# Kernel optimization log

Hardware: AMD Instinct MI355X
Metric: run time of the kernel (lower is better)

Reference implementation:

```python
import jax, jax.numpy as jnp
import numpy as np

NUM_EXPERTS = 3
INPUT_DIM = 1024
HIDDEN_DIM = 4096
OUTPUT_DIM = 1024
ROUTER_HIDDEN = 128
BATCH = 8192


def setup_inputs() -> dict:
    key = jax.random.key(0)
    ks = jax.random.split(key, 6)
    s_in = 1.0 / np.sqrt(INPUT_DIM)
    s_h = 1.0 / np.sqrt(HIDDEN_DIM)
    s_rh = 1.0 / np.sqrt(ROUTER_HIDDEN)
    return {
        "x": jax.random.normal(ks[0], (BATCH, INPUT_DIM), jnp.float32),
        "router_w1": jax.random.normal(ks[1], (INPUT_DIM, ROUTER_HIDDEN), jnp.float32) * s_in,
        "router_b1": jnp.zeros((ROUTER_HIDDEN,), jnp.float32),
        "router_w2": jax.random.normal(ks[2], (ROUTER_HIDDEN, NUM_EXPERTS), jnp.float32) * s_rh,
        "router_b2": jnp.zeros((NUM_EXPERTS,), jnp.float32),
        "expert_w1": jax.random.normal(ks[3], (NUM_EXPERTS, INPUT_DIM, HIDDEN_DIM), jnp.float32) * s_in,
        "expert_b1": jnp.zeros((NUM_EXPERTS, HIDDEN_DIM), jnp.float32),
        "expert_w2": jax.random.normal(ks[4], (NUM_EXPERTS, HIDDEN_DIM, OUTPUT_DIM), jnp.float32) * s_h,
        "expert_b2": jnp.zeros((NUM_EXPERTS, OUTPUT_DIM), jnp.float32),
    }


def reference(x, router_w1, router_b1, router_w2, router_b2,
              expert_w1, expert_b1, expert_w2, expert_b2):
    # Router: MLP -> softmax probs, hard top-1 selection (argmax)
    rh = jax.nn.relu(x @ router_w1 + router_b1)          # [B, 128]
    logits = rh @ router_w2 + router_b2                   # [B, E]
    probs = jax.nn.softmax(logits, axis=-1)
    selected = jnp.argmax(probs, axis=-1)                 # [B] int

    # Per-expert forward on all tokens (dense equivalent of masked dispatch)
    h = jax.nn.relu(jnp.einsum('bi,eih->ebh', x, expert_w1) + expert_b1[:, None, :])  # [E,B,H]
    y = jnp.einsum('ebh,eho->ebo', h, expert_w2) + expert_b2[:, None, :]              # [E,B,O]

    # Scatter-combine: each token takes its selected expert's output
    outputs = jnp.take_along_axis(
        y, selected[None, :, None], axis=0)[0]            # [B, O]

    # routing_stats: tokens per expert
    routing_stats = jnp.bincount(selected, length=NUM_EXPERTS)
    return outputs, routing_stats
```

## Files before the change

kernel.cpp:

```cpp
#include <hip/hip_runtime.h>
#include <hip/hip_bf16.h>

typedef short bf16x8 __attribute__((ext_vector_type(8)));
typedef float f32x4 __attribute__((ext_vector_type(4)));
typedef __attribute__((address_space(1))) const void gconst_t;
typedef __attribute__((address_space(3))) void lds_t;

#define DEVI __device__ __forceinline__

constexpr int BATCH   = 8192;
constexpr int IN_DIM  = 1024;
constexpr int HID     = 4096;
constexpr int OUT_DIM = 1024;
constexpr int NE      = 3;

constexpr size_t XBF_OFF  = 0;
constexpr size_t W1T_OFF  = 16777216;
constexpr size_t W2T_OFF  = W1T_OFF + 25165824;
constexpr size_t H_OFF    = W2T_OFF + 25165824;
constexpr size_t META_OFF = H_OFF + 67108864;

DEVI unsigned short f2bf(float f) {
  __hip_bfloat16 h = __float2bfloat16(f);
  return *reinterpret_cast<unsigned short*>(&h);
}

__global__ __launch_bounds__(256) void prep_kernel(
    const float* __restrict__ x, const float* __restrict__ ew1, const float* __restrict__ ew2,
    const float* __restrict__ rw1, const float* __restrict__ rb1,
    const float* __restrict__ rw2, const float* __restrict__ rb2,
    unsigned short* __restrict__ xb, unsigned short* __restrict__ w1t,
    unsigned short* __restrict__ w2t, int* __restrict__ counts, int* __restrict__ toklist) {
  __shared__ float smem[5184];
  const int b = blockIdx.x;
  const int tid = threadIdx.x;

  if (b < 1024) {
    const int t0 = b * 8;
    float* xs = smem;
    float* rh = smem + 4096;
    const int hcol = tid & 127;
    const int g = tid >> 7;
    float acc[4] = {0.f, 0.f, 0.f, 0.f};
    for (int half = 0; half < 2; half++) {
      __syncthreads();
      {
        const float* xsrc = x + (size_t)t0 * 1024 + half * 512;
        for (int i = tid; i < 1024; i += 256) {
          const int tok = i >> 7, c4 = i & 127;
          *(float4*)&xs[tok * 512 + c4 * 4] =
              *(const float4*)(xsrc + (size_t)tok * 1024 + c4 * 4);
        }
      }
      __syncthreads();
      const int kbase = half * 512;
      for (int k = 0; k < 512; k += 4) {
        const float w0 = rw1[(kbase + k + 0) * 128 + hcol];
        const float w1v = rw1[(kbase + k + 1) * 128 + hcol];
        const float w2v = rw1[(kbase + k + 2) * 128 + hcol];
        const float w3v = rw1[(kbase + k + 3) * 128 + hcol];
#pragma unroll
        for (int tt = 0; tt < 4; tt++) {
          const float4 xv = *(const float4*)&xs[(g * 4 + tt) * 512 + k];
          acc[tt] = fmaf(xv.x, w0, acc[tt]);
          acc[tt] = fmaf(xv.y, w1v, acc[tt]);
          acc[tt] = fmaf(xv.z, w2v, acc[tt]);
          acc[tt] = fmaf(xv.w, w3v, acc[tt]);
        }
      }
    }
    const float bb1 = rb1[hcol];
#pragma unroll
    for (int tt = 0; tt < 4; tt++)
      rh[(g * 4 + tt) * 132 + hcol] = fmaxf(acc[tt] + bb1, 0.f);
    __syncthreads();
    float* lg = smem + 4096 + 8 * 132;
    if (tid < 24) {
      const int t = tid / 3, e = tid % 3;
      float s = rb2[e];
      for (int j = 0; j < 128; j++) s = fmaf(rh[t * 132 + j], rw2[j * 3 + e], s);
      lg[t * 3 + e] = s;
    }
    __syncthreads();
    if (tid < 8) {
      const float l0 = lg[tid * 3], l1 = lg[tid * 3 + 1], l2 = lg[tid * 3 + 2];
      int sel = 0; float m = l0;
      if (l1 > m) { m = l1; sel = 1; }
      if (l2 > m) { m = l2; sel = 2; }
      const int slot = atomicAdd(&counts[sel], 1);
      toklist[sel * BATCH + slot] = t0 + tid;
    }
  } else if (b < 7168) {
    float (*tile)[65] = (float(*)[65])smem;
    const float* src; unsigned short* dst; int R, C, r0, c0;
    if (b < 4096) {
      const int bb = b - 1024, e = bb / 1024, w = bb % 1024;
      src = ew1 + (size_t)e * 1024 * 4096; dst = w1t + (size_t)e * 4096 * 1024;
      R = 1024; C = 4096; r0 = (w & 15) * 64; c0 = (w >> 4) * 64;
    } else {
      const int bb = b - 4096, e = bb / 1024, w = bb % 1024;
      src = ew2 + (size_t)e * 4096 * 1024; dst = w2t + (size_t)e * 1024 * 4096;
      R = 4096; C = 1024; r0 = (w & 63) * 64; c0 = (w >> 6) * 64;
    }
    const int tr = tid >> 4;
    const int tc = (tid & 15) << 2;
#pragma unroll
    for (int i = 0; i < 4; i++) {
      const int r = tr + i * 16;
      const float4 v = *(const float4*)(src + (size_t)(r0 + r) * C + (c0 + tc));
      tile[r][tc + 0] = v.x; tile[r][tc + 1] = v.y; tile[r][tc + 2] = v.z; tile[r][tc + 3] = v.w;
    }
    __syncthreads();
#pragma unroll
    for (int i = 0; i < 4; i++) {
      const int c = tr + i * 16;
      ushort4 o;
      o.x = f2bf(tile[tc + 0][c]);
      o.y = f2bf(tile[tc + 1][c]);
      o.z = f2bf(tile[tc + 2][c]);
      o.w = f2bf(tile[tc + 3][c]);
      *(ushort4*)(dst + (size_t)(c0 + c) * R + (r0 + tc)) = o;
    }
  } else {
    const float4* xv4 = (const float4*)x;
    const int total = BATCH * IN_DIM / 4;
    for (int i = (b - 7168) * 256 + tid; i < total; i += 512 * 256) {
      const float4 v = xv4[i];
      ushort4 o;
      o.x = f2bf(v.x); o.y = f2bf(v.y); o.z = f2bf(v.z); o.w = f2bf(v.w);
      ((ushort4*)xb)[i] = o;
    }
  }
}

template <int MODE>
__global__ __launch_bounds__(512, 2) void moe_gemm(
    const unsigned short* __restrict__ Abase, const unsigned short* __restrict__ Ball,
    const float* __restrict__ biasAll, unsigned short* __restrict__ Hout,
    float* __restrict__ Yout, const int* __restrict__ toklist, const int* __restrict__ counts,
    float* __restrict__ tail) {
  constexpr int N  = (MODE == 0) ? HID : OUT_DIM;
  constexpr int K  = (MODE == 0) ? IN_DIM : HID;
  constexpr int NT = K / 32;

  const int tid = threadIdx.x;
  if (MODE == 0 && blockIdx.x == 0 && blockIdx.y == 0 && tid < NE)
    tail[tid] = (float)counts[tid];

  const int c0 = counts[0], c1 = counts[1], c2 = counts[2];
  const int mb0 = (c0 + 127) >> 7, mb1 = (c1 + 127) >> 7, mb2 = (c2 + 127) >> 7;
  const int bx = blockIdx.x;
  int e, mblk;
  if (bx < mb0) { e = 0; mblk = bx; }
  else if (bx < mb0 + mb1) { e = 1; mblk = bx - mb0; }
  else if (bx < mb0 + mb1 + mb2) { e = 2; mblk = bx - mb0 - mb1; }
  else return;
  const int cnt = (e == 0) ? c0 : (e == 1) ? c1 : c2;
  const int m0 = mblk * 128;
  const int n0 = blockIdx.y * 256;
  const int off_e = (e > 0 ? c0 : 0) + (e > 1 ? c1 : 0);
  const unsigned short* Bmat = Ball + (size_t)e * ((size_t)N * K);
  const float* bias = biasAll + (size_t)e * N;

  __shared__ unsigned short Ab[3][128 * 32];
  __shared__ unsigned short Bb[3][256 * 32];

  const unsigned short* asrc;
  const unsigned short* bsrc[2];
  unsigned aoff, boff[2];
  {
    const unsigned o = (unsigned)tid * 16u;
    const unsigned p = o ^ (((o >> 6) & 3u) << 4);
    const int row = (int)(o >> 6);
    const int kel = (int)((p & 63u) >> 1);
    aoff = o;
    int slot = m0 + row; if (slot > cnt - 1) slot = cnt - 1;
    const size_t arow = (MODE == 0) ? (size_t)toklist[e * BATCH + slot]
                                    : (size_t)(off_e + slot);
    asrc = Abase + arow * K + kel;
  }
#pragma unroll
  for (int l = 0; l < 2; l++) {
    const unsigned o = l * 8192u + (unsigned)tid * 16u;
    const unsigned p = o ^ (((o >> 6) & 3u) << 4);
    const int row = (int)(o >> 6);
    const int kel = (int)((p & 63u) >> 1);
    boff[l] = o;
    bsrc[l] = Bmat + (size_t)(n0 + row) * K + kel;
  }

  f32x4 acc[4][4];
#pragma unroll
  for (int i = 0; i < 4; i++)
#pragma unroll
    for (int j = 0; j < 4; j++) acc[i][j] = {0.f, 0.f, 0.f, 0.f};

  const int lane = tid & 63;
  const int wave = tid >> 6;
  const int wm = (wave >> 2) * 64;
  const int wn = (wave & 3) * 64;
  const int fr = lane & 15;
  const int fc = lane >> 4;

  auto STAGE = [&](int buf, int kofs) {
    __builtin_amdgcn_global_load_lds((gconst_t*)(asrc + kofs),
                                     (lds_t*)((char*)&Ab[buf][0] + aoff), 16, 0, 0);
#pragma unroll
    for (int l = 0; l < 2; l++)
      __builtin_amdgcn_global_load_lds((gconst_t*)(bsrc[l] + kofs),
                                       (lds_t*)((char*)&Bb[buf][0] + boff[l]), 16, 0, 0);
  };

  STAGE(0, 0);
  STAGE(1, 32);

  int cur = 0;
  for (int t = 0; t < NT; ++t) {
    if (t + 1 < NT) asm volatile("s_waitcnt vmcnt(3)" ::: "memory");
    else            asm volatile("s_waitcnt vmcnt(0)" ::: "memory");
    __builtin_amdgcn_sched_barrier(0);
    __builtin_amdgcn_s_barrier();
    __builtin_amdgcn_sched_barrier(0);
    bf16x8 af[4], bv[4];
#pragma unroll
    for (int m = 0; m < 4; m++) {
      const unsigned row = (unsigned)(wm + m * 16 + fr);
      const unsigned addr = ((row << 6) + (unsigned)(fc << 4)) ^ ((row & 3u) << 4);
      af[m] = *(const bf16x8*)((const char*)&Ab[cur][0] + addr);
    }
#pragma unroll
    for (int n = 0; n < 4; n++) {
      const unsigned row = (unsigned)(wn + n * 16 + fr);
      const unsigned addr = ((row << 6) + (unsigned)(fc << 4)) ^ ((row & 3u) << 4);
      bv[n] = *(const bf16x8*)((const char*)&Bb[cur][0] + addr);
    }
    asm volatile("s_waitcnt lgkmcnt(0)" ::: "memory");
    __builtin_amdgcn_sched_barrier(0);
    __builtin_amdgcn_s_setprio(1);
#pragma unroll
    for (int m = 0; m < 4; m++)
#pragma unroll
      for (int n = 0; n < 4; n++)
        acc[m][n] = __builtin_amdgcn_mfma_f32_16x16x32_bf16(af[m], bv[n], acc[m][n], 0, 0, 0);
    __builtin_amdgcn_s_setprio(0);
    if (t + 2 < NT) {
      const int nb = (cur + 2 >= 3) ? cur - 1 : cur + 2;
      STAGE(nb, (t + 2) * 32);
    }
    cur = (cur + 1 == 3) ? 0 : cur + 1;
  }

  const int crow = (lane >> 4) * 4;
  const int ccol = lane & 15;
#pragma unroll
  for (int mi = 0; mi < 4; mi++) {
#pragma unroll
    for (int r = 0; r < 4; r++) {
      const int slot = m0 + wm + mi * 16 + crow + r;
      if (slot >= cnt) continue;
      if (MODE == 0) {
        unsigned short* hrow = Hout + (size_t)(off_e + slot) * HID;
#pragma unroll
        for (int ni = 0; ni < 4; ni++) {
          const int n = n0 + wn + ni * 16 + ccol;
          const float v = acc[mi][ni][r] + bias[n];
          hrow[n] = f2bf(fmaxf(v, 0.f));
        }
      } else {
        const int tok = toklist[e * BATCH + slot];
        float* yrow = Yout + (size_t)tok * OUT_DIM;
#pragma unroll
        for (int ni = 0; ni < 4; ni++) {
          const int n = n0 + wn + ni * 16 + ccol;
          yrow[n] = acc[mi][ni][r] + bias[n];
        }
      }
    }
  }
}

extern "C" void kernel_launch(void* const* d_in, const int* in_sizes, int n_in,
                              void* d_out, int out_size, void* d_ws, size_t ws_size,
                              hipStream_t stream) {
  const float* x   = (const float*)d_in[0];
  const float* rw1 = (const float*)d_in[1];
  const float* rb1 = (const float*)d_in[2];
  const float* rw2 = (const float*)d_in[3];
  const float* rb2 = (const float*)d_in[4];
  const float* ew1 = (const float*)d_in[5];
  const float* eb1 = (const float*)d_in[6];
  const float* ew2 = (const float*)d_in[7];
  const float* eb2 = (const float*)d_in[8];
  float* out = (float*)d_out;

  char* ws = (char*)d_ws;
  unsigned short* xb  = (unsigned short*)(ws + XBF_OFF);
  unsigned short* w1t = (unsigned short*)(ws + W1T_OFF);
  unsigned short* w2t = (unsigned short*)(ws + W2T_OFF);
  unsigned short* h   = (unsigned short*)(ws + H_OFF);
  int* counts  = (int*)(ws + META_OFF);
  int* toklist = counts + 16;
  float* tail = out + (size_t)BATCH * OUT_DIM;

  hipMemsetAsync(counts, 0, 64, stream);
  prep_kernel<<<7680, 256, 0, stream>>>(x, ew1, ew2, rw1, rb1, rw2, rb2,
                                        xb, w1t, w2t, counts, toklist);
  moe_gemm<0><<<dim3(66, 16), 512, 0, stream>>>(xb, w1t, eb1, h, nullptr, toklist, counts, tail);
  moe_gemm<1><<<dim3(66, 4), 512, 0, stream>>>(h, w2t, eb2, nullptr, out, toklist, counts, tail);
}
```

Baseline: 351.9 us.

## Split router into its own kernel with LDS-staged weights and double-buffered loads

The router MLP moves out of the combined prep kernel into a dedicated kernel. Each block now handles 16 tokens instead of 8, and router weight chunks are staged through shared memory with register double-buffering. The goal is to cut repeated global reads of the router weights and stop the router blocks from delaying the weight-transpose blocks. The cost is one extra kernel launch, and the router and weight-conversion work now run back to back rather than interleaved in one grid.

```diff
diff --git a/kernel.cpp b/kernel.cpp
--- a/kernel.cpp
+++ b/kernel.cpp
@@ -25,80 +25,107 @@
   return *reinterpret_cast<unsigned short*>(&h);
 }
 
-__global__ __launch_bounds__(256) void prep_kernel(
+__global__ __launch_bounds__(256) void router_kernel(
+    const float* __restrict__ x, const float* __restrict__ rw1, const float* __restrict__ rb1,
+    const float* __restrict__ rw2, const float* __restrict__ rb2,
+    int* __restrict__ counts, int* __restrict__ toklist) {
+  __shared__ float wbuf[64][128];
+  __shared__ float xbuf[16][64];
+  const int tid = threadIdx.x;
+  const int t0 = blockIdx.x * 16;
+  const int hcol = tid & 127;
+  const int g = tid >> 7;
+
+  float acc[8] = {0.f, 0.f, 0.f, 0.f, 0.f, 0.f, 0.f, 0.f};
+  float4 wA[8], wB[8], xA, xB;
+
+  auto LD = [&](int c, float4* wr, float4& xr) {
+    const int k0 = c * 64;
+#pragma unroll
+    for (int j = 0; j < 8; j++) {
+      const int idx = tid + j * 256;
+      wr[j] = *(const float4*)&rw1[(size_t)(k0 + (idx >> 5)) * 128 + (idx & 31) * 4];
+    }
+    xr = *(const float4*)&x[(size_t)(t0 + (tid >> 4)) * 1024 + k0 + (tid & 15) * 4];
+  };
+  auto ST = [&](const float4* wr, const float4& xr) {
+    float4* wl = (float4*)&wbuf[0][0];
+#pragma unroll
+    for (int j = 0; j < 8; j++) wl[tid + j * 256] = wr[j];
+    ((float4*)&xbuf[0][0])[tid] = xr;
+  };
+  auto FMA_CHUNK = [&]() {
+    for (int kk = 0; kk < 64; kk += 4) {
+      const float w0 = wbuf[kk + 0][hcol];
+      const float w1v = wbuf[kk + 1][hcol];
+      const float w2v = wbuf[kk + 2][hcol];
+      const float w3v = wbuf[kk + 3][hcol];
+#pragma unroll
+      for (int tt = 0; tt < 8; tt++) {
+        const float4 xv = *(const float4*)&xbuf[g * 8 + tt][kk];
+        acc[tt] = fmaf(xv.x, w0, acc[tt]);
+        acc[tt] = fmaf(xv.y, w1v, acc[tt]);
+        acc[tt] = fmaf(xv.z, w2v, acc[tt]);
+        acc[tt] = fmaf(xv.w, w3v, acc[tt]);
+      }
+    }
+  };
+
+  LD(0, wA, xA);
+  for (int c = 0; c < 16; c += 2) {
+    __syncthreads();
+    ST(wA, xA);
+    LD(c + 1, wB, xB);
+    __syncthreads();
+    FMA_CHUNK();
+    __syncthreads();
+    ST(wB, xB);
+    if (c + 2 < 16) LD(c + 2, wA, xA);
+    __syncthreads();
+    FMA_CHUNK();
+  }
+
+  __syncthreads();
+  float* rh = &wbuf[0][0];
+  const float bb1 = rb1[hcol];
+#pragma unroll
+  for (int tt = 0; tt < 8; tt++)
+    rh[(g * 8 + tt) * 132 + hcol] = fmaxf(acc[tt] + bb1, 0.f);
+  __syncthreads();
+  float* lg = &xbuf[0][0];
+  if (tid < 48) {
+    const int t = tid / 3, e = tid % 3;
+    float s = rb2[e];
+    for (int j = 0; j < 128; j++) s = fmaf(rh[t * 132 + j], rw2[j * 3 + e], s);
+    lg[t * 3 + e] = s;
+  }
+  __syncthreads();
+  if (tid < 16) {
+    const float l0 = lg[tid * 3], l1 = lg[tid * 3 + 1], l2 = lg[tid * 3 + 2];
+    int sel = 0; float m = l0;
+    if (l1 > m) { m = l1; sel = 1; }
+    if (l2 > m) { m = l2; sel = 2; }
+    const int slot = atomicAdd(&counts[sel], 1);
+    toklist[sel * BATCH + slot] = t0 + tid;
+  }
+}
+
+__global__ __launch_bounds__(256) void prep2_kernel(
     const float* __restrict__ x, const float* __restrict__ ew1, const float* __restrict__ ew2,
-    const float* __restrict__ rw1, const float* __restrict__ rb1,
-    const float* __restrict__ rw2, const float* __restrict__ rb2,
     unsigned short* __restrict__ xb, unsigned short* __restrict__ w1t,
-    unsigned short* __restrict__ w2t, int* __restrict__ counts, int* __restrict__ toklist) {
-  __shared__ float smem[5184];
+    unsigned short* __restrict__ w2t) {
+  __shared__ float tile[64][65];
   const int b = blockIdx.x;
   const int tid = threadIdx.x;
 
-  if (b < 1024) {
-    const int t0 = b * 8;
-    float* xs = smem;
-    float* rh = smem + 4096;
-    const int hcol = tid & 127;
-    const int g = tid >> 7;
-    float acc[4] = {0.f, 0.f, 0.f, 0.f};
-    for (int half = 0; half < 2; half++) {
-      __syncthreads();
-      {
-        const float* xsrc = x + (size_t)t0 * 1024 + half * 512;
-        for (int i = tid; i < 1024; i += 256) {
-          const int tok = i >> 7, c4 = i & 127;
-          *(float4*)&xs[tok * 512 + c4 * 4] =
-              *(const float4*)(xsrc + (size_t)tok * 1024 + c4 * 4);
-        }
-      }
-      __syncthreads();
-      const int kbase = half * 512;
-      for (int k = 0; k < 512; k += 4) {
-        const float w0 = rw1[(kbase + k + 0) * 128 + hcol];
-        const float w1v = rw1[(kbase + k + 1) * 128 + hcol];
-        const float w2v = rw1[(kbase + k + 2) * 128 + hcol];
-        const float w3v = rw1[(kbase + k + 3) * 128 + hcol];
-#pragma unroll
-        for (int tt = 0; tt < 4; tt++) {
-          const float4 xv = *(const float4*)&xs[(g * 4 + tt) * 512 + k];
-          acc[tt] = fmaf(xv.x, w0, acc[tt]);
-          acc[tt] = fmaf(xv.y, w1v, acc[tt]);
-          acc[tt] = fmaf(xv.z, w2v, acc[tt]);
-          acc[tt] = fmaf(xv.w, w3v, acc[tt]);
-        }
-      }
-    }
-    const float bb1 = rb1[hcol];
-#pragma unroll
-    for (int tt = 0; tt < 4; tt++)
-      rh[(g * 4 + tt) * 132 + hcol] = fmaxf(acc[tt] + bb1, 0.f);
-    __syncthreads();
-    float* lg = smem + 4096 + 8 * 132;
-    if (tid < 24) {
-      const int t = tid / 3, e = tid % 3;
-      float s = rb2[e];
-      for (int j = 0; j < 128; j++) s = fmaf(rh[t * 132 + j], rw2[j * 3 + e], s);
-      lg[t * 3 + e] = s;
-    }
-    __syncthreads();
-    if (tid < 8) {
-      const float l0 = lg[tid * 3], l1 = lg[tid * 3 + 1], l2 = lg[tid * 3 + 2];
-      int sel = 0; float m = l0;
-      if (l1 > m) { m = l1; sel = 1; }
-      if (l2 > m) { m = l2; sel = 2; }
-      const int slot = atomicAdd(&counts[sel], 1);
-      toklist[sel * BATCH + slot] = t0 + tid;
-    }
-  } else if (b < 7168) {
-    float (*tile)[65] = (float(*)[65])smem;
+  if (b < 6144) {
     const float* src; unsigned short* dst; int R, C, r0, c0;
-    if (b < 4096) {
-      const int bb = b - 1024, e = bb / 1024, w = bb % 1024;
+    if (b < 3072) {
+      const int e = b / 1024, w = b % 1024;
       src = ew1 + (size_t)e * 1024 * 4096; dst = w1t + (size_t)e * 4096 * 1024;
       R = 1024; C = 4096; r0 = (w & 15) * 64; c0 = (w >> 4) * 64;
     } else {
-      const int bb = b - 4096, e = bb / 1024, w = bb % 1024;
+      const int bb = b - 3072, e = bb / 1024, w = bb % 1024;
       src = ew2 + (size_t)e * 4096 * 1024; dst = w2t + (size_t)e * 1024 * 4096;
       R = 4096; C = 1024; r0 = (w & 63) * 64; c0 = (w >> 6) * 64;
     }
@@ -124,7 +151,7 @@
   } else {
     const float4* xv4 = (const float4*)x;
     const int total = BATCH * IN_DIM / 4;
-    for (int i = (b - 7168) * 256 + tid; i < total; i += 512 * 256) {
+    for (int i = (b - 6144) * 256 + tid; i < total; i += 512 * 256) {
       const float4 v = xv4[i];
       ushort4 o;
       o.x = f2bf(v.x); o.y = f2bf(v.y); o.z = f2bf(v.z); o.w = f2bf(v.w);
@@ -303,8 +330,8 @@
   float* tail = out + (size_t)BATCH * OUT_DIM;
 
   hipMemsetAsync(counts, 0, 64, stream);
-  prep_kernel<<<7680, 256, 0, stream>>>(x, ew1, ew2, rw1, rb1, rw2, rb2,
-                                        xb, w1t, w2t, counts, toklist);
+  router_kernel<<<512, 256, 0, stream>>>(x, rw1, rb1, rw2, rb2, counts, toklist);
+  prep2_kernel<<<6656, 256, 0, stream>>>(x, ew1, ew2, xb, w1t, w2t);
   moe_gemm<0><<<dim3(66, 16), 512, 0, stream>>>(xb, w1t, eb1, h, nullptr, toklist, counts, tail);
   moe_gemm<1><<<dim3(66, 4), 512, 0, stream>>>(h, w2t, eb2, nullptr, out, toklist, counts, tail);
 }
```

Measured after the change: 746.9 us. 112% more time.
